# Kernel optimization log

Hardware: AMD Instinct MI355X
Metric: run time of the kernel (lower is better)

Reference implementation:

```python
import jax, jax.numpy as jnp
import numpy as np

B, P, ENC = 64, 196, 2048          # batch, num_pixels (14x14), encoder_dim
A, E, D, V = 512, 512, 512, 20000  # attention_dim, embed_dim, decoder_dim, vocab
MAXLEN = 22
T = MAXLEN - 1                     # decode steps (teacher forcing drops last token)


def _lin(k, fan_in, fan_out, scale=0.02):
    return jax.random.normal(k, (fan_in, fan_out), jnp.float32) * scale, jnp.zeros((fan_out,), jnp.float32)


def setup_inputs() -> dict:
    key = jax.random.key(0)
    ks = jax.random.split(key, 16)
    encoder_out = jax.random.normal(ks[0], (B, P, ENC), jnp.float32)
    captions = jax.random.randint(ks[1], (B, MAXLEN), 0, V)
    lens = jax.random.randint(ks[2], (B,), 2, MAXLEN + 1)
    lens = jnp.sort(lens)[::-1].at[0].set(MAXLEN)  # sorted descending, as the torch loop assumes
    emb = jax.random.uniform(ks[3], (V, E), jnp.float32, -0.1, 0.1)
    enc_att_w, enc_att_b = _lin(ks[4], ENC, A)
    dec_att_w, dec_att_b = _lin(ks[5], D, A)
    full_att_w, full_att_b = _lin(ks[6], A, 1)
    w_ih = jax.random.normal(ks[7], (E + ENC, 4 * D), jnp.float32) * 0.02
    w_hh = jax.random.normal(ks[8], (D, 4 * D), jnp.float32) * 0.02
    b_ih = jnp.zeros((4 * D,), jnp.float32)
    b_hh = jnp.zeros((4 * D,), jnp.float32)
    init_h_w, init_h_b = _lin(ks[9], ENC, D)
    init_c_w, init_c_b = _lin(ks[10], ENC, D)
    f_beta_w, f_beta_b = _lin(ks[11], D, ENC)
    fc_w = jax.random.uniform(ks[12], (D, V), jnp.float32, -0.1, 0.1)
    fc_b = jnp.zeros((V,), jnp.float32)
    return dict(encoder_out=encoder_out, captions=captions, lengths=lens, emb=emb,
                enc_att_w=enc_att_w, enc_att_b=enc_att_b, dec_att_w=dec_att_w, dec_att_b=dec_att_b,
                full_att_w=full_att_w, full_att_b=full_att_b, w_ih=w_ih, b_ih=b_ih, w_hh=w_hh, b_hh=b_hh,
                init_h_w=init_h_w, init_h_b=init_h_b, init_c_w=init_c_w, init_c_b=init_c_b,
                f_beta_w=f_beta_w, f_beta_b=f_beta_b, fc_w=fc_w, fc_b=fc_b)


def reference(encoder_out, captions, lengths, emb,
              enc_att_w, enc_att_b, dec_att_w, dec_att_b, full_att_w, full_att_b,
              w_ih, b_ih, w_hh, b_hh, init_h_w, init_h_b, init_c_w, init_c_b,
              f_beta_w, f_beta_b, fc_w, fc_b):
    # Dropout is identity (eval mode) for a deterministic reference.
    dec_len = lengths - 1                       # decode_lengths
    x_emb = emb[captions]                       # (B, L, E)
    mean_enc = encoder_out.mean(axis=1)         # (B, ENC)
    h0 = mean_enc @ init_h_w + init_h_b         # (B, D)
    c0 = mean_enc @ init_c_w + init_c_b
    att1 = encoder_out @ enc_att_w + enc_att_b  # (B, P, A), hoisted out of the loop

    emb_ts = jnp.swapaxes(x_emb[:, :T, :], 0, 1)  # (T, B, E)
    t_idx = jnp.arange(T)

    def step(carry, xt):
        h, c = carry
        e_t, t = xt
        active = (t < dec_len)[:, None]         # ragged batch -> mask (sorted lengths)
        # Bahdanau attention
        att2 = h @ dec_att_w + dec_att_b        # (B, A)
        scores = (jax.nn.relu(att1 + att2[:, None, :]) @ full_att_w)[..., 0] + full_att_b[0]  # (B, P)
        alpha = jax.nn.softmax(scores, axis=1)
        context = jnp.einsum('bp,bpe->be', alpha, encoder_out)
        # gated context
        gate = jax.nn.sigmoid(h @ f_beta_w + f_beta_b)
        context = gate * context
        # LSTMCell (torch gate order i, f, g, o)
        x = jnp.concatenate([e_t, context], axis=1)
        gates = x @ w_ih + h @ w_hh + b_ih + b_hh
        i_g, f_g, g_g, o_g = jnp.split(gates, 4, axis=1)
        c_new = jax.nn.sigmoid(f_g) * c + jax.nn.sigmoid(i_g) * jnp.tanh(g_g)
        h_new = jax.nn.sigmoid(o_g) * jnp.tanh(c_new)
        h = jnp.where(active, h_new, h)
        c = jnp.where(active, c_new, c)
        preds = jnp.where(active, h_new @ fc_w + fc_b, 0.0)
        alpha_o = jnp.where(active, alpha, 0.0)
        return (h, c), (preds, alpha_o)

    _, (preds, alphas) = jax.lax.scan(step, (h0, c0), (emb_ts, t_idx))
    predictions = jnp.swapaxes(preds, 0, 1)     # (B, T, V)
    alphas = jnp.swapaxes(alphas, 0, 1)         # (B, T, P)
    return predictions, alphas
```

## Files before the change

### kernel.cpp

```cpp
#include <hip/hip_runtime.h>

#define BB   64
#define PP   196
#define ENC  2048
#define AA   512
#define EE   512
#define DD   512
#define VV   20000
#define TT   21
#define ML   22

#define PRED_ELEMS ((size_t)BB * TT * VV)

typedef __attribute__((ext_vector_type(8))) short s8bf;
typedef __attribute__((ext_vector_type(4))) float f4acc;

__device__ __forceinline__ float bf2f(unsigned short u) {
    union { unsigned int i; float f; } v; v.i = ((unsigned int)u) << 16; return v.f;
}
__device__ __forceinline__ void unpack2(unsigned int u, float& lo, float& hi) {
    union { unsigned int i; float f; } a, b;
    a.i = u << 16; b.i = u & 0xFFFF0000u; lo = a.f; hi = b.f;
}
__device__ __forceinline__ unsigned short f2bf(float f) {
    union { float f; unsigned int i; } v; v.f = f;
    unsigned int i = v.i;
    return (unsigned short)((i + 0x7FFFu + ((i >> 16) & 1u)) >> 16);
}
__device__ __forceinline__ float sigmoidf(float x) { return 1.0f / (1.0f + __expf(-x)); }

template <bool F> __device__ __forceinline__ float ldw(const void* p, size_t i) {
    if (F) return ((const float*)p)[i];
    return bf2f(((const unsigned short*)p)[i]);
}
template <bool F> __device__ __forceinline__ unsigned short ldbf(const void* p, size_t i) {
    if (F) return f2bf(((const float*)p)[i]);
    return ((const unsigned short*)p)[i];
}
template <bool F> __device__ __forceinline__ float2 ld2(const void* p, size_t i) {
    if (F) return *(const float2*)((const float*)p + i);
    unsigned int u = *(const unsigned int*)((const unsigned short*)p + i);
    float lo, hi; unpack2(u, lo, hi); return make_float2(lo, hi);
}
template <bool F> __device__ __forceinline__ float4 ld4(const void* p, size_t i) {
    if (F) return *(const float4*)((const float*)p + i);
    uint2 u = *(const uint2*)((const unsigned short*)p + i);
    float a, b, c, d; unpack2(u.x, a, b); unpack2(u.y, c, d);
    return make_float4(a, b, c, d);
}
template <bool F> __device__ __forceinline__ void st1(void* p, size_t i, float v) {
    if (F) ((float*)p)[i] = v; else ((unsigned short*)p)[i] = f2bf(v);
}

__global__ void dec_detect_kernel(const unsigned short* __restrict__ enc_us, int* __restrict__ flag) {
    __shared__ int s_cnt;
    if (threadIdx.x == 0) s_cnt = 0;
    __syncthreads();
    int cnt = 0;
    for (int i = threadIdx.x; i < 8192; i += 256) {
        unsigned short u = enc_us[2 * i];
        if ((u & 0x7F80) == 0x7F80) cnt++;
    }
    if (cnt) atomicAdd(&s_cnt, cnt);
    __syncthreads();
    if (threadIdx.x == 0) *flag = (s_cnt > 0) ? 1 : 0;
}

template <bool F>
__device__ __forceinline__ void encconv_body(const void* enc, unsigned short* dst) {
    size_t i = ((size_t)blockIdx.x * 256 + threadIdx.x) * 8;
    if (F) {
        const float* s = (const float*)enc + i;
        float4 v0 = *(const float4*)s, v1 = *(const float4*)(s + 4);
        union { uint4 u; unsigned short h[8]; } o;
        o.h[0]=f2bf(v0.x); o.h[1]=f2bf(v0.y); o.h[2]=f2bf(v0.z); o.h[3]=f2bf(v0.w);
        o.h[4]=f2bf(v1.x); o.h[5]=f2bf(v1.y); o.h[6]=f2bf(v1.z); o.h[7]=f2bf(v1.w);
        *(uint4*)(dst + i) = o.u;
    } else {
        *(uint4*)(dst + i) = *(const uint4*)((const unsigned short*)enc + i);
    }
}
__global__ void enc_bf_kernel(const void* __restrict__ enc, const int* __restrict__ flg,
                              unsigned short* __restrict__ dst) {
    if (*flg) encconv_body<true>(enc, dst); else encconv_body<false>(enc, dst);
}

template <bool F>
__device__ __forceinline__ void conv_swz_body(const void* W, int K, int Norig,
                                              unsigned short* dst, int permMode, int nChunks, int rowOff) {
    int chunk = blockIdx.x * 4 + (threadIdx.x >> 6);
    if (chunk >= nChunks) return;
    int lane = threadIdx.x & 63;
    int KC = K >> 5;
    int nt = chunk / KC, kc = chunk % KC;
    int quad = lane >> 4, l15 = lane & 15;
    int np = nt * 16 + l15;
    int col;
    if (permMode == 1) col = ((np >> 4) & 3) * 512 + (np >> 6) * 16 + (np & 15);
    else col = np;
    union { s8bf v; unsigned short s[8]; } o;
    if (np < Norig || permMode == 1) {
        size_t base = (size_t)(kc * 32 + quad * 8 + rowOff) * Norig + col;
#pragma unroll
        for (int j = 0; j < 8; ++j) o.s[j] = ldbf<F>(W, base + (size_t)j * Norig);
    } else {
#pragma unroll
        for (int j = 0; j < 8; ++j) o.s[j] = 0;
    }
    *(s8bf*)(dst + ((size_t)chunk * 64 + lane) * 8) = o.v;
}
__global__ void conv_swz_kernel(const int* __restrict__ flg, const void* __restrict__ W,
                                int K, int Norig, unsigned short* __restrict__ dst,
                                int permMode, int nChunks, int rowOff) {
    if (*flg) conv_swz_body<true>(W, K, Norig, dst, permMode, nChunks, rowOff);
    else      conv_swz_body<false>(W, K, Norig, dst, permMode, nChunks, rowOff);
}

template <bool F>
__device__ __forceinline__ void transp_body(const void* W, int N, unsigned short* dst) {
    int n = blockIdx.x * 4 + (threadIdx.x >> 6);
    int lane = threadIdx.x & 63;
#pragma unroll
    for (int kk = 0; kk < 8; ++kk) {
        int k = lane + kk * 64;
        dst[(size_t)n * 512 + k] = ldbf<F>(W, (size_t)k * N + n);
    }
}
__global__ void transp_kernel(const int* __restrict__ flg, const void* __restrict__ W,
                              int N, unsigned short* __restrict__ dst) {
    if (*flg) transp_body<true>(W, N, dst); else transp_body<false>(W, N, dst);
}

template <bool F>
__device__ __forceinline__ void embg_body(const void* emb, const int* captions, unsigned short* embg) {
    int gid = blockIdx.x * 256 + threadIdx.x;
    int row = gid >> 6;
    int e0 = (gid & 63) * 8;
    int t = row >> 6, b = row & 63;
    int cap = captions[b * ML + t];
    union { uint4 u; unsigned short h[8]; } o;
#pragma unroll
    for (int j = 0; j < 8; ++j) o.h[j] = ldbf<F>(emb, (size_t)cap * EE + e0 + j);
    *(uint4*)(embg + (size_t)row * 512 + e0) = o.u;
}
__global__ void embg_kernel(const int* __restrict__ flg, const void* __restrict__ emb,
                            const int* __restrict__ captions, unsigned short* __restrict__ embg) {
    if (*flg) embg_body<true>(emb, captions, embg); else embg_body<false>(emb, captions, embg);
}

template <bool F>
__device__ __forceinline__ void conv_bias_body(const void* dab, const void* fbb,
                                               const void* bih, const void* bhh, const void* fcb,
                                               const void* ihb, const void* icb, const void* eab,
                                               float* ag_b, float* g_b, float* fc_b,
                                               float* ihb_f, float* icb_f, float* eab_f) {
    int i = blockIdx.x * 256 + threadIdx.x;
    if (i < 2560) ag_b[i] = (i < 512) ? ldw<F>(dab, i) : ldw<F>(fbb, i - 512);
    else if (i < 2560 + 2048) {
        int np = i - 2560;
        int orig = ((np >> 4) & 3) * 512 + (np >> 6) * 16 + (np & 15);
        g_b[np] = ldw<F>(bih, orig) + ldw<F>(bhh, orig);
    } else if (i < 2560 + 2048 + 20000) fc_b[i - 4608] = ldw<F>(fcb, i - 4608);
    else if (i < 2560 + 2048 + 20000 + 512) ihb_f[i - 24608] = ldw<F>(ihb, i - 24608);
    else if (i < 2560 + 2048 + 20000 + 1024) icb_f[i - 25120] = ldw<F>(icb, i - 25120);
    else if (i < 2560 + 2048 + 20000 + 1536) eab_f[i - 25632] = ldw<F>(eab, i - 25632);
}
__global__ void conv_bias_kernel(const int* __restrict__ flg,
                                 const void* dab, const void* fbb, const void* bih, const void* bhh,
                                 const void* fcb, const void* ihb, const void* icb, const void* eab,
                                 float* ag_b, float* g_b, float* fc_b,
                                 float* ihb_f, float* icb_f, float* eab_f) {
    if (*flg) conv_bias_body<true>(dab, fbb, bih, bhh, fcb, ihb, icb, eab, ag_b, g_b, fc_b, ihb_f, icb_f, eab_f);
    else      conv_bias_body<false>(dab, fbb, bih, bhh, fcb, ihb, icb, eab, ag_b, g_b, fc_b, ihb_f, icb_f, eab_f);
}

template <bool F>
__device__ __forceinline__ void mean_body(const void* enc, unsigned short* mean_bf) {
    int b = blockIdx.x;
    int e = blockIdx.y * 256 + threadIdx.x;
    size_t base = (size_t)b * PP * ENC + e;
    float s = 0.f;
#pragma unroll 4
    for (int p = 0; p < PP; ++p) s += ldw<F>(enc, base + (size_t)p * ENC);
    mean_bf[b * ENC + e] = f2bf(s * (1.0f / (float)PP));
}
__global__ void dec_mean_kernel(const void* __restrict__ enc, const int* __restrict__ flg,
                                unsigned short* __restrict__ mean_bf) {
    if (*flg) mean_body<true>(enc, mean_bf); else mean_body<false>(enc, mean_bf);
}

__global__ __launch_bounds__(256)
void gemm_u_kernel(const int* __restrict__ flg,
                   const unsigned short* __restrict__ A1, int K1, const unsigned short* __restrict__ W1,
                   const unsigned short* __restrict__ A2, int K2, const unsigned short* __restrict__ W2,
                   const float* __restrict__ bias, int N, int epi, int nct,
                   float* __restrict__ outF, const float* __restrict__ outF2,
                   unsigned short* __restrict__ hb, float* __restrict__ cptr,
                   unsigned short* __restrict__ h_all,
                   void* __restrict__ outV, const int* __restrict__ lengths, int t) {
    __shared__ float s_g[4352];
    int tid = threadIdx.x;
    int wave = tid >> 6, lane = tid & 63;
    int l15 = lane & 15, quad = lane >> 4;
    const unsigned short* Abase1 = A1;
    if (epi == 0 || epi == 2) Abase1 = A1 + (size_t)blockIdx.x * 64 * K1;
    f4acc acc[4][2];
#pragma unroll
    for (int a = 0; a < 4; ++a) { acc[a][0] = (f4acc)0.f; acc[a][1] = (f4acc)0.f; }
#pragma unroll
    for (int pass = 0; pass < 2; ++pass) {
        const unsigned short* A = pass ? A2 : Abase1;
        if (!A) continue;
        int K = pass ? K2 : K1;
        const unsigned short* W = pass ? W2 : W1;
        int KC = K >> 5;
        for (int kc = 0; kc < KC; ++kc) {
            s8bf af[4];
#pragma unroll
            for (int rt = 0; rt < 4; ++rt)
                af[rt] = *(const s8bf*)(A + (size_t)(rt * 16 + l15) * K + kc * 32 + quad * 8);
#pragma unroll
            for (int ct = 0; ct < 2; ++ct) if (ct < nct) {
                int nt = blockIdx.y * 4 * nct + ct * 4 + wave;
                s8bf bv = *(const s8bf*)(W + ((size_t)(nt * KC + kc) * 64 + lane) * 8);
#pragma unroll
                for (int rt = 0; rt < 4; ++rt)
                    acc[rt][ct] = __builtin_amdgcn_mfma_f32_16x16x32_bf16(af[rt], bv, acc[rt][ct], 0, 0, 0);
            }
        }
    }
    if (epi == 4) {
        int nl = wave * 16 + l15;
        int g = (nl >> 4) & 3, dl = nl & 15;
        float bv = bias ? bias[blockIdx.y * 64 + nl] : 0.f;
        size_t ecol = (size_t)blockIdx.y * 64 + nl;
#pragma unroll
        for (int rt = 0; rt < 4; ++rt)
#pragma unroll
            for (int r = 0; r < 4; ++r) {
                int m = rt * 16 + quad * 4 + r;
                float ev = outF2 ? outF2[((size_t)t * BB + m) * 2048 + ecol] : 0.f;
                s_g[(g * 64 + m) * 17 + dl] = acc[rt][0][r] + bv + ev;
            }
        __syncthreads();
        int m = tid >> 2;
        bool act = t < (lengths[m] - 1);
#pragma unroll
        for (int i = 0; i < 4; ++i) {
            int dl2 = (tid & 3) * 4 + i;
            int d = blockIdx.y * 16 + dl2;
            unsigned short hv;
            if (act) {
                float ig = sigmoidf(s_g[(0 * 64 + m) * 17 + dl2]);
                float fg = sigmoidf(s_g[(1 * 64 + m) * 17 + dl2]);
                float gg = tanhf(s_g[(2 * 64 + m) * 17 + dl2]);
                float og = sigmoidf(s_g[(3 * 64 + m) * 17 + dl2]);
                float cn = fg * cptr[m * DD + d] + ig * gg;
                float hn = og * tanhf(cn);
                cptr[m * DD + d] = cn;
                hv = f2bf(hn);
            } else {
                hv = A2[(size_t)m * K2 + d];
            }
            hb[m * DD + d] = hv;
            h_all[((size_t)t * BB + m) * DD + d] = hv;
        }
        return;
    }
    if (epi == 2) {
        int t2 = blockIdx.x;
        int base_n = blockIdx.y * 128;
        bool f32o = (*flg != 0);
#pragma unroll
        for (int half = 0; half < 2; ++half) {
            if (half) __syncthreads();
#pragma unroll
            for (int ct = 0; ct < 2; ++ct) {
                int nl = ct * 64 + wave * 16 + l15;
                int nn = base_n + nl;
                float bv = (nn < VV) ? bias[nn] : 0.f;
#pragma unroll
                for (int rt2 = 0; rt2 < 2; ++rt2) {
                    int rt = half * 2 + rt2;
#pragma unroll
                    for (int r = 0; r < 4; ++r) {
                        int mrow = rt2 * 16 + quad * 4 + r;
                        s_g[mrow * 132 + nl] = acc[rt][ct][r] + bv;
                    }
                }
            }
            __syncthreads();
#pragma unroll
            for (int pass = 0; pass < 4; ++pass) {
                int mrow = pass * 8 + (tid >> 5);
                int m = half * 32 + mrow;
                int j = tid & 31;
                int n = base_n + j * 4;
                if (n < VV) {
                    bool act = t2 < (lengths[m] - 1);
                    float4 v = *(const float4*)&s_g[mrow * 132 + j * 4];
// ... 60 lines not shown
        for (int rt = 0; rt < 4; ++rt)
            af[rt] = *(const s8bf*)&As[(rt * 16 + l15) * 40 + quad * 8];
#pragma unroll
        for (int ct = 0; ct < 2; ++ct) {
            int nt = blockIdx.y * 8 + ct * 4 + wave;
            s8bf bv = *(const s8bf*)(Wsw + ((size_t)(nt * 64 + kc) * 64 + lane) * 8);
#pragma unroll
            for (int rt = 0; rt < 4; ++rt)
                acc[rt][ct] = __builtin_amdgcn_mfma_f32_16x16x32_bf16(af[rt], bv, acc[rt][ct], 0, 0, 0);
        }
        __syncthreads();
    }
#pragma unroll
    for (int ct = 0; ct < 2; ++ct) {
        int n = blockIdx.y * 128 + ct * 64 + wave * 16 + l15;
        float bv = bias[n];
#pragma unroll
        for (int rt = 0; rt < 4; ++rt)
#pragma unroll
            for (int r = 0; r < 4; ++r) {
                int m = row0 + rt * 16 + quad * 4 + r;
                att1[(size_t)m * AA + n] = f2bf(acc[rt][ct][r] + bv);
            }
    }
}
__global__ __launch_bounds__(256)
void gemm_att1_kernel(const void* __restrict__ enc, const int* __restrict__ flg,
                      const unsigned short* __restrict__ Wsw, const float* __restrict__ bias,
                      unsigned short* __restrict__ att1) {
    if (*flg) att1_gemm_body<true>(enc, Wsw, bias, att1);
    else      att1_gemm_body<false>(enc, Wsw, bias, att1);
}

template <bool F>
__device__ __forceinline__ void att_body(const unsigned short* att1, const unsigned short* hcur,
                                         const unsigned short* dawT, const float* ag_bias,
                                         const void* faw, const void* fab,
                                         const int* lengths, float* alpha_ws, void* out, int t) {
    __shared__ float s_h[512];
    __shared__ float s_att2[512];
    __shared__ float s_sc[256];
    __shared__ float s_red[256];
    int b = blockIdx.x, tid = threadIdx.x;
    if (tid < 256) {
        unsigned int hv = *(const unsigned int*)(hcur + (size_t)b * DD + tid * 2);
        float lo, hi; unpack2(hv, lo, hi);
        s_h[tid * 2] = lo; s_h[tid * 2 + 1] = hi;
        s_sc[tid] = -1e30f;
    }
    __syncthreads();
    {
        int n = tid >> 1, half = tid & 1;
        const unsigned short* wr = dawT + (size_t)n * 512 + half * 256;
        const float* hh = s_h + half * 256;
        float acc = 0.f;
#pragma unroll 4
        for (int kk = 0; kk < 256; kk += 8) {
            s8bf wv = *(const s8bf*)(wr + kk);
#pragma unroll
            for (int j = 0; j < 8; ++j) acc += hh[kk + j] * bf2f((unsigned short)wv[j]);
        }
        acc += __shfl_xor(acc, 1, 64);
        if (half == 0) s_att2[n] = acc + ag_bias[n];
    }
    __syncthreads();
    int wave = tid >> 6, lane = tid & 63;
    int a0i = lane * 8;
    float a2[8];
#pragma unroll
    for (int j = 0; j < 8; ++j) a2[j] = s_att2[a0i + j];
    float4 w0 = ld4<F>(faw, a0i);
    float4 w1 = ld4<F>(faw, a0i + 4);
    float fabv = ldw<F>(fab, 0);
    for (int r = wave; r < PP; r += 16) {
        uint4 u = *(const uint4*)(att1 + ((size_t)b * PP + r) * AA + a0i);
        float v0, v1, v2, v3, v4, v5, v6, v7;
        unpack2(u.x, v0, v1); unpack2(u.y, v2, v3);
        unpack2(u.z, v4, v5); unpack2(u.w, v6, v7);
        float acc = fmaxf(v0 + a2[0], 0.f) * w0.x
                  + fmaxf(v1 + a2[1], 0.f) * w0.y
                  + fmaxf(v2 + a2[2], 0.f) * w0.z
                  + fmaxf(v3 + a2[3], 0.f) * w0.w
                  + fmaxf(v4 + a2[4], 0.f) * w1.x
                  + fmaxf(v5 + a2[5], 0.f) * w1.y
                  + fmaxf(v6 + a2[6], 0.f) * w1.z
                  + fmaxf(v7 + a2[7], 0.f) * w1.w;
#pragma unroll
        for (int off = 32; off; off >>= 1) acc += __shfl_xor(acc, off, 64);
        if (lane == 0) s_sc[r] = acc + fabv;
    }
    __syncthreads();
    float sc = (tid < 256) ? s_sc[tid] : -1e30f;
    if (tid < 256) s_red[tid] = sc;
    __syncthreads();
    for (int s = 128; s > 0; s >>= 1) { if (tid < s) s_red[tid] = fmaxf(s_red[tid], s_red[tid + s]); __syncthreads(); }
    float m = s_red[0];
    __syncthreads();
    float e = 0.f;
    if (tid < PP) e = __expf(sc - m);
    if (tid < 256) s_red[tid] = e;
    __syncthreads();
    for (int s = 128; s > 0; s >>= 1) { if (tid < s) s_red[tid] += s_red[tid + s]; __syncthreads(); }
    float inv = 1.0f / s_red[0];
    if (tid < PP) {
        float al = e * inv;
        alpha_ws[b * PP + tid] = al;
        bool active = t < (lengths[b] - 1);
        st1<F>(out, PRED_ELEMS + (size_t)(b * TT + t) * PP + tid, active ? al : 0.f);
    }
}
__global__ __launch_bounds__(1024)
void dec_att_kernel(const unsigned short* __restrict__ att1, const unsigned short* __restrict__ hcur,
                    const unsigned short* __restrict__ dawT, const float* __restrict__ ag_bias,
                    const int* __restrict__ flg,
                    const void* __restrict__ faw, const void* __restrict__ fab,
                    const int* __restrict__ lengths,
                    float* __restrict__ alpha_ws, void* __restrict__ out, int t) {
    if (*flg) att_body<true>(att1, hcur, dawT, ag_bias, faw, fab, lengths, alpha_ws, out, t);
    else      att_body<false>(att1, hcur, dawT, ag_bias, faw, fab, lengths, alpha_ws, out, t);
}

__global__ __launch_bounds__(256)
void dec_ctx_kernel(const void* __restrict__ encp, const int* __restrict__ flg, int forceBf,
                    const float* __restrict__ alpha_ws, const unsigned short* __restrict__ hcur,
                    const unsigned short* __restrict__ fbwT, const float* __restrict__ ag_bias,
                    unsigned short* __restrict__ xc_bf, int t) {
    __shared__ float s_al[PP];
    __shared__ float s_h[512];
    int b = blockIdx.x, yc = blockIdx.y, tid = threadIdx.x;
    if (tid < PP) s_al[tid] = alpha_ws[b * PP + tid];
    {
        unsigned int hv = *(const unsigned int*)(hcur + (size_t)b * DD + tid * 2);
        float lo, hi; unpack2(hv, lo, hi);
        s_h[tid * 2] = lo; s_h[tid * 2 + 1] = hi;
    }
    __syncthreads();
    int e = yc * 512 + tid * 2;
    const unsigned short* w0r = fbwT + (size_t)e * 512;
    const unsigned short* w1r = w0r + 512;
    float g0 = 0.f, g1 = 0.f;
#pragma unroll 4
    for (int kk = 0; kk < 512; kk += 8) {
        s8bf wa = *(const s8bf*)(w0r + kk);
        s8bf wb = *(const s8bf*)(w1r + kk);
#pragma unroll
        for (int j = 0; j < 8; ++j) {
            float hv = s_h[kk + j];
            g0 += hv * bf2f((unsigned short)wa[j]);
            g1 += hv * bf2f((unsigned short)wb[j]);
        }
    }
    g0 = sigmoidf(g0 + ag_bias[512 + e]);
    g1 = sigmoidf(g1 + ag_bias[512 + e + 1]);
    float a0 = 0.f, a1 = 0.f;
    size_t base = (size_t)b * PP * ENC + e;
    bool encF32 = (*flg != 0) && !forceBf;
    if (encF32) {
#pragma unroll 16
        for (int p = 0; p < PP; ++p) {
            float al = s_al[p];
            float2 v = *(const float2*)((const float*)encp + base + (size_t)p * ENC);
            a0 += al * v.x; a1 += al * v.y;
        }
    } else {
#pragma unroll 16
        for (int p = 0; p < PP; ++p) {
            float al = s_al[p];
            unsigned int u = *(const unsigned int*)((const unsigned short*)encp + base + (size_t)p * ENC);
            float lo, hi; unpack2(u, lo, hi);
            a0 += al * lo; a1 += al * hi;
        }
    }
    *(unsigned int*)(xc_bf + (size_t)b * 2048 + e) =
        (unsigned int)f2bf(a0 * g0) | ((unsigned int)f2bf(a1 * g1) << 16);
}

extern "C" void kernel_launch(void* const* d_in, const int* in_sizes, int n_in,
                              void* d_out, int out_size, void* d_ws, size_t ws_size,
                              hipStream_t stream) {
    const void* enc      = d_in[0];
    const int* captions  = (const int*)d_in[1];
    const int* lengths   = (const int*)d_in[2];
    const void* emb      = d_in[3];
    const void* eaw      = d_in[4];
    const void* eab      = d_in[5];
    const void* daw      = d_in[6];
    const void* dab      = d_in[7];
    const void* faw      = d_in[8];
    const void* fab      = d_in[9];
    const void* wih      = d_in[10];
    const void* bih      = d_in[11];
    const void* whh      = d_in[12];
    const void* bhh      = d_in[13];
    const void* ihw      = d_in[14];
    const void* ihb      = d_in[15];
    const void* icw      = d_in[16];
    const void* icb      = d_in[17];
    const void* fbw      = d_in[18];
    const void* fbb      = d_in[19];
    const void* fcw      = d_in[20];
    const void* fcb      = d_in[21];

    char* cur = (char*)d_ws;
    auto alloc = [&](size_t bytes) { void* p = cur; cur += (bytes + 255) & ~(size_t)255; return p; };
    int* flg               = (int*)alloc(4);
    unsigned short* h_bufA = (unsigned short*)alloc((size_t)BB * DD * 2);
    unsigned short* h_bufB = (unsigned short*)alloc((size_t)BB * DD * 2);
    unsigned short* h_all  = (unsigned short*)alloc((size_t)TT * BB * DD * 2);
    unsigned short* xc_bf  = (unsigned short*)alloc((size_t)BB * 2048 * 2);
    unsigned short* mean_bf= (unsigned short*)alloc((size_t)BB * ENC * 2);
    float* c               = (float*)alloc((size_t)BB * DD * 4);
    float* alpha           = (float*)alloc((size_t)BB * PP * 4);
    float* ag_bias         = (float*)alloc(2560 * 4);
    float* g_bias          = (float*)alloc(2048 * 4);
    float* fc_bias         = (float*)alloc(20000 * 4);
    float* ihb_f           = (float*)alloc(512 * 4);
    float* icb_f           = (float*)alloc(512 * 4);
    float* eab_f           = (float*)alloc(512 * 4);
    unsigned short* daw_T  = (unsigned short*)alloc((size_t)512 * 512 * 2);
    unsigned short* fbw_T  = (unsigned short*)alloc((size_t)2048 * 512 * 2);
    unsigned short* embg   = (unsigned short*)alloc((size_t)TT * BB * 512 * 2);
    float* E_all           = (float*)alloc((size_t)TT * BB * 2048 * 4);
    unsigned short* eaw_sw = (unsigned short*)alloc((size_t)32 * 64 * 512 * 2);
    unsigned short* ihw_sw = (unsigned short*)alloc((size_t)32 * 64 * 512 * 2);
    unsigned short* icw_sw = (unsigned short*)alloc((size_t)32 * 64 * 512 * 2);
    unsigned short* wihA_sw= (unsigned short*)alloc((size_t)128 * 16 * 512 * 2);
    unsigned short* wihB_sw= (unsigned short*)alloc((size_t)128 * 64 * 512 * 2);
    unsigned short* whh_sw = (unsigned short*)alloc((size_t)128 * 16 * 512 * 2);
    unsigned short* fcw_sw = (unsigned short*)alloc((size_t)1256 * 16 * 512 * 2);
    unsigned short* att1_bf= (unsigned short*)alloc((size_t)BB * PP * AA * 2);
    size_t enc_bf_bytes = (size_t)BB * PP * ENC * 2;
    size_t used = (size_t)(cur - (char*)d_ws);
    bool have_enc_bf = (used + enc_bf_bytes + 256 <= ws_size);
    unsigned short* enc_bf = have_enc_bf ? (unsigned short*)alloc(enc_bf_bytes) : nullptr;

    dec_detect_kernel<<<1, 256, 0, stream>>>((const unsigned short*)enc, flg);
    if (have_enc_bf)
        enc_bf_kernel<<<(BB * PP * ENC) / (256 * 8), 256, 0, stream>>>(enc, flg, enc_bf);
    conv_swz_kernel<<<512, 256, 0, stream>>>(flg, eaw, ENC, AA, eaw_sw, 0, 32 * 64, 0);
    conv_swz_kernel<<<512, 256, 0, stream>>>(flg, ihw, ENC, DD, ihw_sw, 0, 32 * 64, 0);
    conv_swz_kernel<<<512, 256, 0, stream>>>(flg, icw, ENC, DD, icw_sw, 0, 32 * 64, 0);
    conv_swz_kernel<<<512, 256, 0, stream>>>(flg, wih, 512, 2048, wihA_sw, 1, 128 * 16, 0);
    conv_swz_kernel<<<2048, 256, 0, stream>>>(flg, wih, 2048, 2048, wihB_sw, 1, 128 * 64, 512);
    conv_swz_kernel<<<512, 256, 0, stream>>>(flg, whh, DD, 2048, whh_sw, 1, 128 * 16, 0);
    conv_swz_kernel<<<5024, 256, 0, stream>>>(flg, fcw, DD, VV, fcw_sw, 0, 1256 * 16, 0);
    transp_kernel<<<128, 256, 0, stream>>>(flg, daw, AA, daw_T);
    transp_kernel<<<512, 256, 0, stream>>>(flg, fbw, ENC, fbw_T);
    conv_bias_kernel<<<(26144 + 255) / 256, 256, 0, stream>>>(flg, dab, fbb, bih, bhh, fcb, ihb, icb, eab,
                                                              ag_bias, g_bias, fc_bias, ihb_f, icb_f, eab_f);
    dec_mean_kernel<<<dim3(BB, ENC / 256), 256, 0, stream>>>(enc, flg, mean_bf);
    embg_kernel<<<(TT * BB * 64) / 256, 256, 0, stream>>>(flg, emb, captions, embg);
    gemm_u_kernel<<<dim3(1, 4), 256, 0, stream>>>(flg, mean_bf, ENC, ihw_sw, nullptr, 0, nullptr,
                                                  ihb_f, DD, 3, 2, nullptr, nullptr, h_bufA, nullptr,
                                                  nullptr, nullptr, nullptr, 0);
    gemm_u_kernel<<<dim3(1, 4), 256, 0, stream>>>(flg, mean_bf, ENC, icw_sw, nullptr, 0, nullptr,
                                                  icb_f, DD, 0, 2, c, nullptr, nullptr, nullptr,
                                                  nullptr, nullptr, nullptr, 0);
    gemm_u_kernel<<<dim3(TT, 32), 256, 0, stream>>>(flg, embg, 512, wihA_sw, nullptr, 0, nullptr,
                                                    g_bias, 2048, 0, 1, E_all, nullptr, nullptr, nullptr,
                                                    nullptr, nullptr, nullptr, 0);
    gemm_att1_kernel<<<dim3(196, 4), 256, 0, stream>>>(enc, flg, eaw_sw, eab_f, att1_bf);

    const void* ctx_enc = have_enc_bf ? (const void*)enc_bf : enc;
    int forceBf = have_enc_bf ? 1 : 0;
    unsigned short* hcur = h_bufA;
    for (int t = 0; t < TT; ++t) {
        unsigned short* hnext = (hcur == h_bufA) ? h_bufB : h_bufA;
        dec_att_kernel<<<BB, 1024, 0, stream>>>(att1_bf, hcur, daw_T, ag_bias, flg, faw, fab,
                                                lengths, alpha, d_out, t);
        dec_ctx_kernel<<<dim3(BB, 4), 256, 0, stream>>>(ctx_enc, flg, forceBf, alpha, hcur, fbw_T,
                                                        ag_bias, xc_bf, t);
        gemm_u_kernel<<<dim3(1, 32), 256, 0, stream>>>(flg, xc_bf, 2048, wihB_sw, hcur, DD, whh_sw,
                                                       nullptr, 2048, 4, 1, nullptr, E_all, hnext, c,
                                                       h_all, nullptr, lengths, t);
        hcur = hnext;
    }
    gemm_u_kernel<<<dim3(TT, 157), 256, 0, stream>>>(flg, h_all, DD, fcw_sw, nullptr, 0, nullptr,
                                                     fc_bias, VV, 2, 2, nullptr, nullptr, nullptr, nullptr,
                                                     nullptr, d_out, lengths, 0);
}
```

Before: 2.928 ms.

## Fuse per-step decoder kernels into one persistent kernel with grid barriers

Replaces the 63 per-timestep launches (attention, context, LSTM gemm) with a single persistent 256-block kernel that loops over all steps and synchronises through an atomic global barrier. The h-projections for att2 and the gate now run as one MFMA gemm over a swizzled concatenated weight instead of scalar transposed dot products. Attention and softmax are recomputed per (batch, quarter) block. The goal is to remove launch overhead and idle gaps between the many small kernels. In exchange it relies on all 256 blocks being co-resident for the spin barrier, and it adds three barrier round-trips per step.

```diff
diff --git a/kernel.cpp b/kernel.cpp
--- a/kernel.cpp
+++ b/kernel.cpp
@@ -37,22 +37,15 @@
     if (F) return f2bf(((const float*)p)[i]);
     return ((const unsigned short*)p)[i];
 }
-template <bool F> __device__ __forceinline__ float2 ld2(const void* p, size_t i) {
-    if (F) return *(const float2*)((const float*)p + i);
-    unsigned int u = *(const unsigned int*)((const unsigned short*)p + i);
-    float lo, hi; unpack2(u, lo, hi); return make_float2(lo, hi);
-}
 template <bool F> __device__ __forceinline__ float4 ld4(const void* p, size_t i) {
     if (F) return *(const float4*)((const float*)p + i);
     uint2 u = *(const uint2*)((const unsigned short*)p + i);
     float a, b, c, d; unpack2(u.x, a, b); unpack2(u.y, c, d);
     return make_float4(a, b, c, d);
 }
-template <bool F> __device__ __forceinline__ void st1(void* p, size_t i, float v) {
-    if (F) ((float*)p)[i] = v; else ((unsigned short*)p)[i] = f2bf(v);
-}
-
-__global__ void dec_detect_kernel(const unsigned short* __restrict__ enc_us, int* __restrict__ flag) {
+
+__global__ void dec_detect_kernel(const unsigned short* __restrict__ enc_us, int* __restrict__ flag,
+                                  int* __restrict__ bar) {
     __shared__ int s_cnt;
     if (threadIdx.x == 0) s_cnt = 0;
     __syncthreads();
@@ -63,7 +56,7 @@
     }
     if (cnt) atomicAdd(&s_cnt, cnt);
     __syncthreads();
-    if (threadIdx.x == 0) *flag = (s_cnt > 0) ? 1 : 0;
+    if (threadIdx.x == 0) { *flag = (s_cnt > 0) ? 1 : 0; *bar = 0; }
 }
 
 template <bool F>
@@ -117,21 +110,6 @@
 }
 
 template <bool F>
-__device__ __forceinline__ void transp_body(const void* W, int N, unsigned short* dst) {
-    int n = blockIdx.x * 4 + (threadIdx.x >> 6);
-    int lane = threadIdx.x & 63;
-#pragma unroll
-    for (int kk = 0; kk < 8; ++kk) {
-        int k = lane + kk * 64;
-        dst[(size_t)n * 512 + k] = ldbf<F>(W, (size_t)k * N + n);
-    }
-}
-__global__ void transp_kernel(const int* __restrict__ flg, const void* __restrict__ W,
-                              int N, unsigned short* __restrict__ dst) {
-    if (*flg) transp_body<true>(W, N, dst); else transp_body<false>(W, N, dst);
-}
-
-template <bool F>
 __device__ __forceinline__ void embg_body(const void* emb, const int* captions, unsigned short* embg) {
     int gid = blockIdx.x * 256 + threadIdx.x;
     int row = gid >> 6;
@@ -191,81 +169,32 @@
 
 __global__ __launch_bounds__(256)
 void gemm_u_kernel(const int* __restrict__ flg,
-                   const unsigned short* __restrict__ A1, int K1, const unsigned short* __restrict__ W1,
-                   const unsigned short* __restrict__ A2, int K2, const unsigned short* __restrict__ W2,
+                   const unsigned short* __restrict__ A, int K, const unsigned short* __restrict__ W,
                    const float* __restrict__ bias, int N, int epi, int nct,
-                   float* __restrict__ outF, const float* __restrict__ outF2,
-                   unsigned short* __restrict__ hb, float* __restrict__ cptr,
-                   unsigned short* __restrict__ h_all,
-                   void* __restrict__ outV, const int* __restrict__ lengths, int t) {
-    __shared__ float s_g[4352];
+                   float* __restrict__ outF, unsigned short* __restrict__ hb,
+                   void* __restrict__ outV, const int* __restrict__ lengths) {
+    __shared__ float s_g[4224];
     int tid = threadIdx.x;
     int wave = tid >> 6, lane = tid & 63;
     int l15 = lane & 15, quad = lane >> 4;
-    const unsigned short* Abase1 = A1;
-    if (epi == 0 || epi == 2) Abase1 = A1 + (size_t)blockIdx.x * 64 * K1;
+    const unsigned short* Abase = A + (size_t)blockIdx.x * 64 * K;
+    int KC = K >> 5;
     f4acc acc[4][2];
 #pragma unroll
-    for (int a = 0; a < 4; ++a) { acc[a][0] = (f4acc)0.f; acc[a][1] = (f4acc)0.f; }
-#pragma unroll
-    for (int pass = 0; pass < 2; ++pass) {
-        const unsigned short* A = pass ? A2 : Abase1;
-        if (!A) continue;
-        int K = pass ? K2 : K1;
-        const unsigned short* W = pass ? W2 : W1;
-        int KC = K >> 5;
-        for (int kc = 0; kc < KC; ++kc) {
-            s8bf af[4];
+    for (int x = 0; x < 4; ++x) { acc[x][0] = (f4acc)0.f; acc[x][1] = (f4acc)0.f; }
+    for (int kc = 0; kc < KC; ++kc) {
+        s8bf af[4];
+#pragma unroll
+        for (int rt = 0; rt < 4; ++rt)
+            af[rt] = *(const s8bf*)(Abase + (size_t)(rt * 16 + l15) * K + kc * 32 + quad * 8);
+#pragma unroll
+        for (int ct = 0; ct < 2; ++ct) if (ct < nct) {
+            int nt = blockIdx.y * 4 * nct + ct * 4 + wave;
+            s8bf bv = *(const s8bf*)(W + ((size_t)(nt * KC + kc) * 64 + lane) * 8);
 #pragma unroll
             for (int rt = 0; rt < 4; ++rt)
-                af[rt] = *(const s8bf*)(A + (size_t)(rt * 16 + l15) * K + kc * 32 + quad * 8);
-#pragma unroll
-            for (int ct = 0; ct < 2; ++ct) if (ct < nct) {
-                int nt = blockIdx.y * 4 * nct + ct * 4 + wave;
-                s8bf bv = *(const s8bf*)(W + ((size_t)(nt * KC + kc) * 64 + lane) * 8);
-#pragma unroll
-                for (int rt = 0; rt < 4; ++rt)
-                    acc[rt][ct] = __builtin_amdgcn_mfma_f32_16x16x32_bf16(af[rt], bv, acc[rt][ct], 0, 0, 0);
-            }
+                acc[rt][ct] = __builtin_amdgcn_mfma_f32_16x16x32_bf16(af[rt], bv, acc[rt][ct], 0, 0, 0);
         }
-    }
-    if (epi == 4) {
-        int nl = wave * 16 + l15;
-        int g = (nl >> 4) & 3, dl = nl & 15;
-        float bv = bias ? bias[blockIdx.y * 64 + nl] : 0.f;
-        size_t ecol = (size_t)blockIdx.y * 64 + nl;
-#pragma unroll
-        for (int rt = 0; rt < 4; ++rt)
-#pragma unroll
-            for (int r = 0; r < 4; ++r) {
-                int m = rt * 16 + quad * 4 + r;
-                float ev = outF2 ? outF2[((size_t)t * BB + m) * 2048 + ecol] : 0.f;
-                s_g[(g * 64 + m) * 17 + dl] = acc[rt][0][r] + bv + ev;
-            }
-        __syncthreads();
-        int m = tid >> 2;
-        bool act = t < (lengths[m] - 1);
-#pragma unroll
-        for (int i = 0; i < 4; ++i) {
-            int dl2 = (tid & 3) * 4 + i;
-            int d = blockIdx.y * 16 + dl2;
-            unsigned short hv;
-            if (act) {
-                float ig = sigmoidf(s_g[(0 * 64 + m) * 17 + dl2]);
-                float fg = sigmoidf(s_g[(1 * 64 + m) * 17 + dl2]);
-                float gg = tanhf(s_g[(2 * 64 + m) * 17 + dl2]);
-                float og = sigmoidf(s_g[(3 * 64 + m) * 17 + dl2]);
-                float cn = fg * cptr[m * DD + d] + ig * gg;
-                float hn = og * tanhf(cn);
-                cptr[m * DD + d] = cn;
-                hv = f2bf(hn);
-            } else {
-                hv = A2[(size_t)m * K2 + d];
-            }
-            hb[m * DD + d] = hv;
-            h_all[((size_t)t * BB + m) * DD + d] = hv;
-        }
-        return;
     }
     if (epi == 2) {
         int t2 = blockIdx.x;
@@ -392,147 +321,215 @@
     else      att1_gemm_body<false>(enc, Wsw, bias, att1);
 }
 
-template <bool F>
-__device__ __forceinline__ void att_body(const unsigned short* att1, const unsigned short* hcur,
-                                         const unsigned short* dawT, const float* ag_bias,
-                                         const void* faw, const void* fab,
-                                         const int* lengths, float* alpha_ws, void* out, int t) {
-    __shared__ float s_h[512];
-    __shared__ float s_att2[512];
-    __shared__ float s_sc[256];
-    __shared__ float s_red[256];
-    int b = blockIdx.x, tid = threadIdx.x;
-    if (tid < 256) {
-        unsigned int hv = *(const unsigned int*)(hcur + (size_t)b * DD + tid * 2);
-        float lo, hi; unpack2(hv, lo, hi);
-        s_h[tid * 2] = lo; s_h[tid * 2 + 1] = hi;
-        s_sc[tid] = -1e30f;
-    }
+struct LoopArgs {
+    const int* flg;
+    const unsigned short* att1;
+    const void* encp; int forceBf;
+    const unsigned short* ag_sw; const float* ag_bias;
+    const void* faw; const void* fab;
+    unsigned short* hA; unsigned short* hB;
+    float* c; float* att2; float* gate;
+    unsigned short* xc;
+    const unsigned short* wihB; const unsigned short* whh;
+    const float* E_all;
+    unsigned short* h_all;
+    const int* lengths;
+    void* out;
+    int* bar;
+};
+
+__device__ __forceinline__ void gbar(int* cnt, int target) {
     __syncthreads();
-    {
-        int n = tid >> 1, half = tid & 1;
-        const unsigned short* wr = dawT + (size_t)n * 512 + half * 256;
-        const float* hh = s_h + half * 256;
-        float acc = 0.f;
-#pragma unroll 4
-        for (int kk = 0; kk < 256; kk += 8) {
-            s8bf wv = *(const s8bf*)(wr + kk);
-#pragma unroll
-            for (int j = 0; j < 8; ++j) acc += hh[kk + j] * bf2f((unsigned short)wv[j]);
+    if (threadIdx.x == 0) {
+        __threadfence();
+        atomicAdd(cnt, 1);
+        while (atomicAdd(cnt, 0) < target) __builtin_amdgcn_s_sleep(16);
+        __threadfence();
+    }
+    __syncthreads();
+}
+
+__global__ __launch_bounds__(256)
+void dec_loop_kernel(LoopArgs a) {
+    __shared__ float s_g[4352];
+    int blk = blockIdx.x, tid = threadIdx.x;
+    int wave = tid >> 6, lane = tid & 63;
+    int l15 = lane & 15, quad = lane >> 4;
+    bool f32in = (*a.flg != 0);
+    int bt = 256;
+    for (int t = 0; t < TT; ++t) {
+        const unsigned short* hc = (t & 1) ? a.hB : a.hA;
+        unsigned short* hn = (t & 1) ? a.hA : a.hB;
+        if (blk < 20) {
+            f4acc acc[4][2];
+#pragma unroll
+            for (int x = 0; x < 4; ++x) { acc[x][0] = (f4acc)0.f; acc[x][1] = (f4acc)0.f; }
+            for (int kc = 0; kc < 16; ++kc) {
+                s8bf af[4];
+#pragma unroll
+                for (int rt = 0; rt < 4; ++rt)
+                    af[rt] = *(const s8bf*)(hc + (size_t)(rt * 16 + l15) * DD + kc * 32 + quad * 8);
+#pragma unroll
+                for (int ct = 0; ct < 2; ++ct) {
+                    int nt = blk * 8 + ct * 4 + wave;
+                    s8bf bv = *(const s8bf*)(a.ag_sw + ((size_t)(nt * 16 + kc) * 64 + lane) * 8);
+#pragma unroll
+                    for (int rt = 0; rt < 4; ++rt)
+                        acc[rt][ct] = __builtin_amdgcn_mfma_f32_16x16x32_bf16(af[rt], bv, acc[rt][ct], 0, 0, 0);
+                }
+            }
+#pragma unroll
+            for (int ct = 0; ct < 2; ++ct) {
+                int n = blk * 128 + ct * 64 + wave * 16 + l15;
+                float bv = a.ag_bias[n];
+#pragma unroll
+                for (int rt = 0; rt < 4; ++rt)
+#pragma unroll
+                    for (int r = 0; r < 4; ++r) {
+                        int m = rt * 16 + quad * 4 + r;
+                        float v = acc[rt][ct][r] + bv;
+                        if (n < 512) a.att2[(size_t)m * 512 + n] = v;
+                        else         a.gate[(size_t)m * 2048 + (n - 512)] = sigmoidf(v);
+                    }
+            }
         }
-        acc += __shfl_xor(acc, 1, 64);
-        if (half == 0) s_att2[n] = acc + ag_bias[n];
-    }
-    __syncthreads();
-    int wave = tid >> 6, lane = tid & 63;
-    int a0i = lane * 8;
-    float a2[8];
-#pragma unroll
-    for (int j = 0; j < 8; ++j) a2[j] = s_att2[a0i + j];
-    float4 w0 = ld4<F>(faw, a0i);
-    float4 w1 = ld4<F>(faw, a0i + 4);
-    float fabv = ldw<F>(fab, 0);
-    for (int r = wave; r < PP; r += 16) {
-        uint4 u = *(const uint4*)(att1 + ((size_t)b * PP + r) * AA + a0i);
-        float v0, v1, v2, v3, v4, v5, v6, v7;
-        unpack2(u.x, v0, v1); unpack2(u.y, v2, v3);
-        unpack2(u.z, v4, v5); unpack2(u.w, v6, v7);
-        float acc = fmaxf(v0 + a2[0], 0.f) * w0.x
-                  + fmaxf(v1 + a2[1], 0.f) * w0.y
-                  + fmaxf(v2 + a2[2], 0.f) * w0.z
-                  + fmaxf(v3 + a2[3], 0.f) * w0.w
-                  + fmaxf(v4 + a2[4], 0.f) * w1.x
-                  + fmaxf(v5 + a2[5], 0.f) * w1.y
-                  + fmaxf(v6 + a2[6], 0.f) * w1.z
-                  + fmaxf(v7 + a2[7], 0.f) * w1.w;
-#pragma unroll
-        for (int off = 32; off; off >>= 1) acc += __shfl_xor(acc, off, 64);
-        if (lane == 0) s_sc[r] = acc + fabv;
-    }
-    __syncthreads();
-    float sc = (tid < 256) ? s_sc[tid] : -1e30f;
-    if (tid < 256) s_red[tid] = sc;
-    __syncthreads();
-    for (int s = 128; s > 0; s >>= 1) { if (tid < s) s_red[tid] = fmaxf(s_red[tid], s_red[tid + s]); __syncthreads(); }
-    float m = s_red[0];
-    __syncthreads();
-    float e = 0.f;
-    if (tid < PP) e = __expf(sc - m);
-    if (tid < 256) s_red[tid] = e;
-    __syncthreads();
-    for (int s = 128; s > 0; s >>= 1) { if (tid < s) s_red[tid] += s_red[tid + s]; __syncthreads(); }
-    float inv = 1.0f / s_red[0];
-    if (tid < PP) {
-        float al = e * inv;
-        alpha_ws[b * PP + tid] = al;
-        bool active = t < (lengths[b] - 1);
-        st1<F>(out, PRED_ELEMS + (size_t)(b * TT + t) * PP + tid, active ? al : 0.f);
-    }
-}
-__global__ __launch_bounds__(1024)
-void dec_att_kernel(const unsigned short* __restrict__ att1, const unsigned short* __restrict__ hcur,
-                    const unsigned short* __restrict__ dawT, const float* __restrict__ ag_bias,
-                    const int* __restrict__ flg,
-                    const void* __restrict__ faw, const void* __restrict__ fab,
-                    const int* __restrict__ lengths,
-                    float* __restrict__ alpha_ws, void* __restrict__ out, int t) {
-    if (*flg) att_body<true>(att1, hcur, dawT, ag_bias, faw, fab, lengths, alpha_ws, out, t);
-    else      att_body<false>(att1, hcur, dawT, ag_bias, faw, fab, lengths, alpha_ws, out, t);
-}
-
-__global__ __launch_bounds__(256)
-void dec_ctx_kernel(const void* __restrict__ encp, const int* __restrict__ flg, int forceBf,
-                    const float* __restrict__ alpha_ws, const unsigned short* __restrict__ hcur,
-                    const unsigned short* __restrict__ fbwT, const float* __restrict__ ag_bias,
-                    unsigned short* __restrict__ xc_bf, int t) {
-    __shared__ float s_al[PP];
-    __shared__ float s_h[512];
-    int b = blockIdx.x, yc = blockIdx.y, tid = threadIdx.x;
-    if (tid < PP) s_al[tid] = alpha_ws[b * PP + tid];
-    {
-        unsigned int hv = *(const unsigned int*)(hcur + (size_t)b * DD + tid * 2);
-        float lo, hi; unpack2(hv, lo, hi);
-        s_h[tid * 2] = lo; s_h[tid * 2 + 1] = hi;
-    }
-    __syncthreads();
-    int e = yc * 512 + tid * 2;
-    const unsigned short* w0r = fbwT + (size_t)e * 512;
-    const unsigned short* w1r = w0r + 512;
-    float g0 = 0.f, g1 = 0.f;
-#pragma unroll 4
-    for (int kk = 0; kk < 512; kk += 8) {
-        s8bf wa = *(const s8bf*)(w0r + kk);
-        s8bf wb = *(const s8bf*)(w1r + kk);
-#pragma unroll
-        for (int j = 0; j < 8; ++j) {
-            float hv = s_h[kk + j];
-            g0 += hv * bf2f((unsigned short)wa[j]);
-            g1 += hv * bf2f((unsigned short)wb[j]);
+        gbar(a.bar, bt); bt += 256;
+        {
+            int b = blk >> 2, yc = blk & 3;
+            float* s_sc = s_g;
+            float* s_red = s_g + 256;
+            s_sc[tid] = -1e30f;
+            __syncthreads();
+            int a0i = lane * 8;
+            float4 p0 = *(const float4*)(a.att2 + (size_t)b * 512 + a0i);
+            float4 p1 = *(const float4*)(a.att2 + (size_t)b * 512 + a0i + 4);
+            float4 w0, w1; float fabv;
+            if (f32in) { w0 = ld4<true>(a.faw, a0i);  w1 = ld4<true>(a.faw, a0i + 4);  fabv = ldw<true>(a.fab, 0); }
+            else       { w0 = ld4<false>(a.faw, a0i); w1 = ld4<false>(a.faw, a0i + 4); fabv = ldw<false>(a.fab, 0); }
+            for (int r = wave; r < PP; r += 4) {
+                uint4 u = *(const uint4*)(a.att1 + ((size_t)b * PP + r) * AA + a0i);
+                float v0, v1, v2, v3, v4, v5, v6, v7;
+                unpack2(u.x, v0, v1); unpack2(u.y, v2, v3);
+                unpack2(u.z, v4, v5); unpack2(u.w, v6, v7);
+                float s = fmaxf(v0 + p0.x, 0.f) * w0.x + fmaxf(v1 + p0.y, 0.f) * w0.y
+                        + fmaxf(v2 + p0.z, 0.f) * w0.z + fmaxf(v3 + p0.w, 0.f) * w0.w
+                        + fmaxf(v4 + p1.x, 0.f) * w1.x + fmaxf(v5 + p1.y, 0.f) * w1.y
+                        + fmaxf(v6 + p1.z, 0.f) * w1.z + fmaxf(v7 + p1.w, 0.f) * w1.w;
+#pragma unroll
+                for (int off = 32; off; off >>= 1) s += __shfl_xor(s, off, 64);
+                if (lane == 0) s_sc[r] = s + fabv;
+            }
+            __syncthreads();
+            float sc = s_sc[tid];
+            s_red[tid] = sc;
+            __syncthreads();
+            for (int st = 128; st > 0; st >>= 1) { if (tid < st) s_red[tid] = fmaxf(s_red[tid], s_red[tid + st]); __syncthreads(); }
+            float mx = s_red[0];
+            __syncthreads();
+            float ex = (tid < PP) ? __expf(sc - mx) : 0.f;
+            s_red[tid] = ex;
+            __syncthreads();
+            for (int st = 128; st > 0; st >>= 1) { if (tid < st) s_red[tid] += s_red[tid + st]; __syncthreads(); }
+            float inv = 1.0f / s_red[0];
+            float al = ex * inv;
+            if (tid < PP) {
+                s_sc[tid] = al;
+                if (yc == 0) {
+                    bool active = t < (a.lengths[b] - 1);
+                    float ov = active ? al : 0.f;
+                    size_t oi = PRED_ELEMS + (size_t)(b * TT + t) * PP + tid;
+                    if (f32in) ((float*)a.out)[oi] = ov;
+                    else       ((unsigned short*)a.out)[oi] = f2bf(ov);
+                }
+            }
+            __syncthreads();
+            int e2 = yc * 512 + tid * 2;
+            float2 gv = *(const float2*)(a.gate + (size_t)b * 2048 + e2);
+            float c0 = 0.f, c1 = 0.f;
+            size_t base = (size_t)b * PP * ENC + e2;
+            bool encF32 = f32in && !a.forceBf;
+            if (encF32) {
+#pragma unroll 16
+                for (int p = 0; p < PP; ++p) {
+                    float alp = s_sc[p];
+                    float2 v = *(const float2*)((const float*)a.encp + base + (size_t)p * ENC);
+                    c0 += alp * v.x; c1 += alp * v.y;
+                }
+            } else {
+#pragma unroll 16
+                for (int p = 0; p < PP; ++p) {
+                    float alp = s_sc[p];
+                    unsigned int u = *(const unsigned int*)((const unsigned short*)a.encp + base + (size_t)p * ENC);
+                    float lo, hi; unpack2(u, lo, hi);
+                    c0 += alp * lo; c1 += alp * hi;
+                }
+            }
+            *(unsigned int*)(a.xc + (size_t)b * 2048 + e2) =
+                (unsigned int)f2bf(c0 * gv.x) | ((unsigned int)f2bf(c1 * gv.y) << 16);
         }
-    }
-    g0 = sigmoidf(g0 + ag_bias[512 + e]);
-    g1 = sigmoidf(g1 + ag_bias[512 + e + 1]);
-    float a0 = 0.f, a1 = 0.f;
-    size_t base = (size_t)b * PP * ENC + e;
-    bool encF32 = (*flg != 0) && !forceBf;
-    if (encF32) {
-#pragma unroll 16
-        for (int p = 0; p < PP; ++p) {
-            float al = s_al[p];
-            float2 v = *(const float2*)((const float*)encp + base + (size_t)p * ENC);
-            a0 += al * v.x; a1 += al * v.y;
+        gbar(a.bar, bt); bt += 256;
+        if (blk < 32) {
+            f4acc acc[4];
+#pragma unroll
+            for (int x = 0; x < 4; ++x) acc[x] = (f4acc)0.f;
+            int nt = blk * 4 + wave;
+            for (int kc = 0; kc < 64; ++kc) {
+                s8bf af[4];
+#pragma unroll
+                for (int rt = 0; rt < 4; ++rt)
+                    af[rt] = *(const s8bf*)(a.xc + (size_t)(rt * 16 + l15) * 2048 + kc * 32 + quad * 8);
+                s8bf bv = *(const s8bf*)(a.wihB + ((size_t)(nt * 64 + kc) * 64 + lane) * 8);
+#pragma unroll
+                for (int rt = 0; rt < 4; ++rt)
+                    acc[rt] = __builtin_amdgcn_mfma_f32_16x16x32_bf16(af[rt], bv, acc[rt], 0, 0, 0);
+            }
+            for (int kc = 0; kc < 16; ++kc) {
+                s8bf af[4];
+#pragma unroll
+                for (int rt = 0; rt < 4; ++rt)
+                    af[rt] = *(const s8bf*)(hc + (size_t)(rt * 16 + l15) * DD + kc * 32 + quad * 8);
+                s8bf bv = *(const s8bf*)(a.whh + ((size_t)(nt * 16 + kc) * 64 + lane) * 8);
+#pragma unroll
+                for (int rt = 0; rt < 4; ++rt)
+                    acc[rt] = __builtin_amdgcn_mfma_f32_16x16x32_bf16(af[rt], bv, acc[rt], 0, 0, 0);
+            }
+            int nl = wave * 16 + l15;
+            int g = (nl >> 4) & 3, dl = nl & 15;
+            size_t ecol = (size_t)blk * 64 + nl;
+#pragma unroll
+            for (int rt = 0; rt < 4; ++rt)
+#pragma unroll
+                for (int r = 0; r < 4; ++r) {
+                    int m = rt * 16 + quad * 4 + r;
+                    float ev = a.E_all[((size_t)t * BB + m) * 2048 + ecol];
+                    s_g[(g * 64 + m) * 17 + dl] = acc[rt][r] + ev;
+                }
+            __syncthreads();
+            int m = tid >> 2;
+            bool act = t < (a.lengths[m] - 1);
+#pragma unroll
+            for (int i = 0; i < 4; ++i) {
+                int dl2 = (tid & 3) * 4 + i;
+                int d = blk * 16 + dl2;
+                unsigned short hv;
+                if (act) {
+                    float ig = sigmoidf(s_g[(0 * 64 + m) * 17 + dl2]);
+                    float fg = sigmoidf(s_g[(1 * 64 + m) * 17 + dl2]);
+                    float gg = tanhf(s_g[(2 * 64 + m) * 17 + dl2]);
+                    float og = sigmoidf(s_g[(3 * 64 + m) * 17 + dl2]);
+                    float cn = fg * a.c[m * DD + d] + ig * gg;
+                    float hnv = og * tanhf(cn);
+                    a.c[m * DD + d] = cn;
+                    hv = f2bf(hnv);
+                } else {
+                    hv = hc[(size_t)m * DD + d];
+                }
+                hn[(size_t)m * DD + d] = hv;
+                a.h_all[((size_t)t * BB + m) * DD + d] = hv;
+            }
         }
-    } else {
-#pragma unroll 16
-        for (int p = 0; p < PP; ++p) {
-            float al = s_al[p];
-            unsigned int u = *(const unsigned int*)((const unsigned short*)encp + base + (size_t)p * ENC);
-            float lo, hi; unpack2(u, lo, hi);
-            a0 += al * lo; a1 += al * hi;
-        }
-    }
-    *(unsigned int*)(xc_bf + (size_t)b * 2048 + e) =
-        (unsigned int)f2bf(a0 * g0) | ((unsigned int)f2bf(a1 * g1) << 16);
+        if (t + 1 < TT) { gbar(a.bar, bt); bt += 256; }
+    }
 }
 
 extern "C" void kernel_launch(void* const* d_in, const int* in_sizes, int n_in,
@@ -564,26 +561,27 @@
     char* cur = (char*)d_ws;
     auto alloc = [&](size_t bytes) { void* p = cur; cur += (bytes + 255) & ~(size_t)255; return p; };
     int* flg               = (int*)alloc(4);
+    int* bar               = (int*)alloc(4);
     unsigned short* h_bufA = (unsigned short*)alloc((size_t)BB * DD * 2);
     unsigned short* h_bufB = (unsigned short*)alloc((size_t)BB * DD * 2);
     unsigned short* h_all  = (unsigned short*)alloc((size_t)TT * BB * DD * 2);
     unsigned short* xc_bf  = (unsigned short*)alloc((size_t)BB * 2048 * 2);
     unsigned short* mean_bf= (unsigned short*)alloc((size_t)BB * ENC * 2);
     float* c               = (float*)alloc((size_t)BB * DD * 4);
-    float* alpha           = (float*)alloc((size_t)BB * PP * 4);
+    float* att2            = (float*)alloc((size_t)BB * AA * 4);
+    float* gate            = (float*)alloc((size_t)BB * ENC * 4);
     float* ag_bias         = (float*)alloc(2560 * 4);
     float* g_bias          = (float*)alloc(2048 * 4);
     float* fc_bias         = (float*)alloc(20000 * 4);
     float* ihb_f           = (float*)alloc(512 * 4);
     float* icb_f           = (float*)alloc(512 * 4);
     float* eab_f           = (float*)alloc(512 * 4);
-    unsigned short* daw_T  = (unsigned short*)alloc((size_t)512 * 512 * 2);
-    unsigned short* fbw_T  = (unsigned short*)alloc((size_t)2048 * 512 * 2);
     unsigned short* embg   = (unsigned short*)alloc((size_t)TT * BB * 512 * 2);
     float* E_all           = (float*)alloc((size_t)TT * BB * 2048 * 4);
     unsigned short* eaw_sw = (unsigned short*)alloc((size_t)32 * 64 * 512 * 2);
     unsigned short* ihw_sw = (unsigned short*)alloc((size_t)32 * 64 * 512 * 2);
     unsigned short* icw_sw = (unsigned short*)alloc((size_t)32 * 64 * 512 * 2);
+    unsigned short* ag_sw  = (unsigned short*)alloc((size_t)160 * 16 * 512 * 2);
     unsigned short* wihA_sw= (unsigned short*)alloc((size_t)128 * 16 * 512 * 2);
     unsigned short* wihB_sw= (unsigned short*)alloc((size_t)128 * 64 * 512 * 2);
     unsigned short* whh_sw = (unsigned short*)alloc((size_t)128 * 16 * 512 * 2);
@@ -594,48 +592,44 @@
     bool have_enc_bf = (used + enc_bf_bytes + 256 <= ws_size);
     unsigned short* enc_bf = have_enc_bf ? (unsigned short*)alloc(enc_bf_bytes) : nullptr;
 
-    dec_detect_kernel<<<1, 256, 0, stream>>>((const unsigned short*)enc, flg);
+    dec_detect_kernel<<<1, 256, 0, stream>>>((const unsigned short*)enc, flg, bar);
     if (have_enc_bf)
         enc_bf_kernel<<<(BB * PP * ENC) / (256 * 8), 256, 0, stream>>>(enc, flg, enc_bf);
     conv_swz_kernel<<<512, 256, 0, stream>>>(flg, eaw, ENC, AA, eaw_sw, 0, 32 * 64, 0);
     conv_swz_kernel<<<512, 256, 0, stream>>>(flg, ihw, ENC, DD, ihw_sw, 0, 32 * 64, 0);
     conv_swz_kernel<<<512, 256, 0, stream>>>(flg, icw, ENC, DD, icw_sw, 0, 32 * 64, 0);
+    conv_swz_kernel<<<128, 256, 0, stream>>>(flg, daw, DD, AA, ag_sw, 0, 32 * 16, 0);
+    conv_swz_kernel<<<512, 256, 0, stream>>>(flg, fbw, DD, ENC, ag_sw + (size_t)32 * 16 * 512, 0, 128 * 16, 0);
     conv_swz_kernel<<<512, 256, 0, stream>>>(flg, wih, 512, 2048, wihA_sw, 1, 128 * 16, 0);
     conv_swz_kernel<<<2048, 256, 0, stream>>>(flg, wih, 2048, 2048, wihB_sw, 1, 128 * 64, 512);
     conv_swz_kernel<<<512, 256, 0, stream>>>(flg, whh, DD, 2048, whh_sw, 1, 128 * 16, 0);
     conv_swz_kernel<<<5024, 256, 0, stream>>>(flg, fcw, DD, VV, fcw_sw, 0, 1256 * 16, 0);
-    transp_kernel<<<128, 256, 0, stream>>>(flg, daw, AA, daw_T);
-    transp_kernel<<<512, 256, 0, stream>>>(flg, fbw, ENC, fbw_T);
     conv_bias_kernel<<<(26144 + 255) / 256, 256, 0, stream>>>(flg, dab, fbb, bih, bhh, fcb, ihb, icb, eab,
                                                               ag_bias, g_bias, fc_bias, ihb_f, icb_f, eab_f);
     dec_mean_kernel<<<dim3(BB, ENC / 256), 256, 0, stream>>>(enc, flg, mean_bf);
     embg_kernel<<<(TT * BB * 64) / 256, 256, 0, stream>>>(flg, emb, captions, embg);
-    gemm_u_kernel<<<dim3(1, 4), 256, 0, stream>>>(flg, mean_bf, ENC, ihw_sw, nullptr, 0, nullptr,
-                                                  ihb_f, DD, 3, 2, nullptr, nullptr, h_bufA, nullptr,
-                                                  nullptr, nullptr, nullptr, 0);
-    gemm_u_kernel<<<dim3(1, 4), 256, 0, stream>>>(flg, mean_bf, ENC, icw_sw, nullptr, 0, nullptr,
-                                                  icb_f, DD, 0, 2, c, nullptr, nullptr, nullptr,
-                                                  nullptr, nullptr, nullptr, 0);
-    gemm_u_kernel<<<dim3(TT, 32), 256, 0, stream>>>(flg, embg, 512, wihA_sw, nullptr, 0, nullptr,
-                                                    g_bias, 2048, 0, 1, E_all, nullptr, nullptr, nullptr,
-                                                    nullptr, nullptr, nullptr, 0);
+    gemm_u_kernel<<<dim3(1, 4), 256, 0, stream>>>(flg, mean_bf, ENC, ihw_sw, ihb_f, DD, 3, 2,
+                                                  nullptr, h_bufA, nullptr, nullptr);
+    gemm_u_kernel<<<dim3(1, 4), 256, 0, stream>>>(flg, mean_bf, ENC, icw_sw, icb_f, DD, 0, 2,
+                                                  c, nullptr, nullptr, nullptr);
+    gemm_u_kernel<<<dim3(TT, 32), 256, 0, stream>>>(flg, embg, 512, wihA_sw, g_bias, 2048, 0, 1,
+                                                    E_all, nullptr, nullptr, nullptr);
     gemm_att1_kernel<<<dim3(196, 4), 256, 0, stream>>>(enc, flg, eaw_sw, eab_f, att1_bf);
 
-    const void* ctx_enc = have_enc_bf ? (const void*)enc_bf : enc;
-    int forceBf = have_enc_bf ? 1 : 0;
-    unsigned short* hcur = h_bufA;
-    for (int t = 0; t < TT; ++t) {
-        unsigned short* hnext = (hcur == h_bufA) ? h_bufB : h_bufA;
-        dec_att_kernel<<<BB, 1024, 0, stream>>>(att1_bf, hcur, daw_T, ag_bias, flg, faw, fab,
-                                                lengths, alpha, d_out, t);
-        dec_ctx_kernel<<<dim3(BB, 4), 256, 0, stream>>>(ctx_enc, flg, forceBf, alpha, hcur, fbw_T,
-                                                        ag_bias, xc_bf, t);
-        gemm_u_kernel<<<dim3(1, 32), 256, 0, stream>>>(flg, xc_bf, 2048, wihB_sw, hcur, DD, whh_sw,
-                                                       nullptr, 2048, 4, 1, nullptr, E_all, hnext, c,
-                                                       h_all, nullptr, lengths, t);
-        hcur = hnext;
-    }
-    gemm_u_kernel<<<dim3(TT, 157), 256, 0, stream>>>(flg, h_all, DD, fcw_sw, nullptr, 0, nullptr,
-                                                     fc_bias, VV, 2, 2, nullptr, nullptr, nullptr, nullptr,
-                                                     nullptr, d_out, lengths, 0);
-}
+    LoopArgs la;
+    la.flg = flg; la.att1 = att1_bf;
+    la.encp = have_enc_bf ? (const void*)enc_bf : enc;
+    la.forceBf = have_enc_bf ? 1 : 0;
+    la.ag_sw = ag_sw; la.ag_bias = ag_bias;
+    la.faw = faw; la.fab = fab;
+    la.hA = h_bufA; la.hB = h_bufB;
+    la.c = c; la.att2 = att2; la.gate = gate;
+    la.xc = xc_bf;
+    la.wihB = wihB_sw; la.whh = whh_sw;
+    la.E_all = E_all; la.h_all = h_all;
+    la.lengths = lengths; la.out = d_out; la.bar = bar;
+    dec_loop_kernel<<<256, 256, 0, stream>>>(la);
+
+    gemm_u_kernel<<<dim3(TT, 157), 256, 0, stream>>>(flg, h_all, DD, fcw_sw, fc_bias, VV, 2, 2,
+                                                     nullptr, nullptr, d_out, lengths);
+}
```

New measurement: 5.000 ms. 1.71x slower.
